# Optimization experiments

Hardware: AMD Instinct MI355X
Metric: run time of the kernel (lower is better)

Reference implementation:

```python
import jax, jax.numpy as jnp
import numpy as np
from jax import lax

HEADS = 8
DK = 128
DV = 128  # attention_channels


def circ_conv(x, w):
    # Conv2d with circular padding that preserves spatial size (odd kernel).
    k = w.shape[2]
    p = k // 2
    if p > 0:
        x = jnp.pad(x, ((0, 0), (0, 0), (p, p), (p, p)), mode='wrap')
    return lax.conv_general_dilated(x, w, (1, 1), 'VALID',
                                    dimension_numbers=('NCHW', 'OIHW', 'NCHW'))


def setup_inputs() -> dict:
    key = jax.random.key(0)
    k1, k2, k3, k4 = jax.random.split(key, 4)
    x = jax.random.normal(k1, (4, 128, 48, 48), dtype=jnp.float32)
    w_init = jax.random.normal(k2, (128, 128, 3, 3), dtype=jnp.float32) * 0.03
    w_qkv = jax.random.normal(k3, (384, 128, 3, 3), dtype=jnp.float32) * 0.03
    w_out = jax.random.normal(k4, (128, 128, 1, 1), dtype=jnp.float32) * 0.1
    return {"x": x, "w_init": w_init, "w_qkv": w_qkv, "w_out": w_out}


def reference(x, w_init, w_qkv, w_out):
    out = circ_conv(x, w_init)               # (b, out_ch - dv, h, w)
    b, _, H, W = out.shape
    N = H * W
    dk_h = DK // HEADS
    dv_h = DV // HEADS

    qkv = circ_conv(x, w_qkv)                # (b, 2*dk+dv, h, w)
    q, k, v = jnp.split(qkv, [DK, 2 * DK], axis=1)

    scale = dk_h ** (-0.5)
    fq = q.reshape(b, HEADS, dk_h, N) * scale
    fk = k.reshape(b, HEADS, dk_h, N)
    fv = v.reshape(b, HEADS, dv_h, N)

    logits = jnp.einsum('bhdn,bhdm->bhnm', fq, fk)     # (b,H,N,N)
    weights = jax.nn.softmax(logits, axis=-1)
    attn = jnp.einsum('bhnm,bhdm->bhnd', weights, fv)  # (b,H,N,dv_h)

    # Faithful to torch: raw reshape (b,H,N,dv_h) -> (b,H,dv_h,h,w)
    attn = attn.reshape(b, HEADS, dv_h, H, W)
    attn = attn.reshape(b, HEADS * dv_h, H, W)
    attn = circ_conv(attn, w_out)
    return jnp.concatenate([out, attn], axis=1)
```

## Files before the change

kernel.cpp:

```cpp
#include <hip/hip_runtime.h>

typedef __attribute__((ext_vector_type(8))) short short8;
typedef __attribute__((ext_vector_type(4))) short shortx4;
typedef __attribute__((ext_vector_type(4))) float floatx4;
typedef __attribute__((ext_vector_type(4))) _Float16 half4;
typedef __attribute__((ext_vector_type(2))) _Float16 half2v;

__device__ __forceinline__ short bf16_short(float f) {
    unsigned u = __builtin_bit_cast(unsigned, f);
    u = (u + 0x7fff + ((u >> 16) & 1)) >> 16;
    return (short)u;
}

__device__ __forceinline__ float fast_exp2(float x) {
#if __has_builtin(__builtin_amdgcn_exp2f)
    return __builtin_amdgcn_exp2f(x);
#else
    return __expf(x * 0.6931471805599453f);
#endif
}

__device__ __forceinline__ half4 pk4(float p0, float p1, float p2, float p3) {
#if __has_builtin(__builtin_amdgcn_cvt_pkrtz)
    half2v lo = __builtin_bit_cast(half2v, __builtin_amdgcn_cvt_pkrtz(p0, p1));
    half2v hi = __builtin_bit_cast(half2v, __builtin_amdgcn_cvt_pkrtz(p2, p3));
    half4 o; o[0] = lo[0]; o[1] = lo[1]; o[2] = hi[0]; o[3] = hi[1];
    return o;
#else
    half4 o; o[0] = (_Float16)p0; o[1] = (_Float16)p1;
    o[2] = (_Float16)p2; o[3] = (_Float16)p3;
    return o;
#endif
}

__global__ __launch_bounds__(256) void transform_w(
    const float* __restrict__ wi, const float* __restrict__ wq,
    const float* __restrict__ wo, const float* __restrict__ x,
    short* __restrict__ Wt, short* __restrict__ Wot, short* __restrict__ Xt)
{
    if (blockIdx.x < 2368) {
        int idx = blockIdx.x * 256 + threadIdx.x;
        if (idx < 589824) {
            int j  = idx & 7;
            int t1 = idx >> 3;
            int co = t1 & 127;
            int t2 = t1 >> 7;
            int chunk = t2 & 15;
            int t3 = t2 >> 4;
            int cog = t3 & 3;
            int tap = t3 >> 2;
            int ci = chunk * 8 + j;
            float v;
            if (cog == 0) v = wi[(co * 128 + ci) * 9 + tap];
            else          v = wq[((((cog - 1) * 128) + co) * 128 + ci) * 9 + tap];
            Wt[idx] = bf16_short(v);
        } else {
            int i2 = idx - 589824;
            int j  = i2 & 7;
            int co = (i2 >> 3) & 127;
            int chunk = i2 >> 10;
            int ci = chunk * 8 + j;
            Wot[i2] = bf16_short(wo[co * 128 + ci]);
        }
    } else {
        int xid = (blockIdx.x - 2368) * 256 + threadIdx.x;
        int col   = xid % 48;
        int row   = (xid / 48) % 48;
        int chunk = (xid / 2304) % 16;
        int b     = xid / 36864;
        const float* xs = x + ((b * 128 + chunk * 8) * 48 + row) * 48 + col;
        short8 o;
        #pragma unroll
        for (int j = 0; j < 8; ++j) o[j] = bf16_short(xs[j * 2304]);
        *(short8*)&Xt[(size_t)xid * 8] = o;
    }
}

__global__ __launch_bounds__(512) void conv_main(
    const short* __restrict__ Xt, const short* __restrict__ Wt,
    float* __restrict__ dout, _Float16* __restrict__ qT,
    _Float16* __restrict__ kT, _Float16* __restrict__ vA)
{
    const int y   = blockIdx.x;
    const int cog = blockIdx.y;
    const int b   = blockIdx.z;

    __shared__ short Xs[16 * 3 * 48 * 8];

    const int t = threadIdx.x;
    const int wave = t >> 6, lane = t & 63, quad = lane >> 4, l16 = lane & 15;
    const int wv = wave & 3;
    const int kk0 = (wave >> 2) * 2;

    const short* wA = Wt + (size_t)cog * 16384 + (wv * 32 + l16) * 8;

    short8 A[2][4];
    #pragma unroll
    for (int kk = 0; kk < 2; ++kk) {
        int chA = (kk0 + kk) * 4 + quad;
        A[0][kk * 2 + 0] = *(const short8*)(wA + chA * 1024);
        A[0][kk * 2 + 1] = *(const short8*)(wA + chA * 1024 + 128);
    }

    {
        const short* xtb = Xt + (size_t)b * 16 * 48 * 48 * 8;
        #pragma unroll
        for (int it = 0; it < 5; ++it) {
            int w = it * 512 + t;
            if (w < 2304) {
                int col   = w % 48;
                int row3  = (w / 48) % 3;
                int chunk = w / 144;
                int rowg  = y + row3 - 1;
                rowg = (rowg < 0) ? rowg + 48 : (rowg >= 48 ? rowg - 48 : rowg);
                short8 v = *(const short8*)&xtb[((chunk * 48 + rowg) * 48 + col) * 8];
                *(short8*)&Xs[((chunk * 3 + row3) * 48 + col) * 8] = v;
            }
        }
    }

    floatx4 acc[2][3];
    #pragma unroll
    for (int i = 0; i < 2; ++i)
        #pragma unroll
        for (int jn = 0; jn < 3; ++jn) acc[i][jn] = (floatx4){0.f, 0.f, 0.f, 0.f};

    __syncthreads();

    #pragma unroll
    for (int tap = 0; tap < 9; ++tap) {
        const int cur = tap & 1;
        if (tap < 8) {
            const short* wn = wA + (tap + 1) * 65536;
            #pragma unroll
            for (int kk = 0; kk < 2; ++kk) {
                int chA = (kk0 + kk) * 4 + quad;
                A[cur ^ 1][kk * 2 + 0] = *(const short8*)(wn + chA * 1024);
                A[cur ^ 1][kk * 2 + 1] = *(const short8*)(wn + chA * 1024 + 128);
            }
        }

        const int dy = tap / 3, dx = tap % 3;
        int colw[3];
        #pragma unroll
        for (int nt = 0; nt < 3; ++nt) {
            int c = nt * 16 + l16 + dx - 1;
            c = (c < 0) ? c + 48 : (c >= 48 ? c - 48 : c);
            colw[nt] = c;
        }

        #pragma unroll
        for (int kk = 0; kk < 2; ++kk) {
            int chA = (kk0 + kk) * 4 + quad;
            short8 a0 = A[cur][kk * 2 + 0];
            short8 a1 = A[cur][kk * 2 + 1];
            #pragma unroll
            for (int nt = 0; nt < 3; ++nt) {
                short8 bf = *(const short8*)&Xs[((chA * 3 + dy) * 48 + colw[nt]) * 8];
                acc[0][nt] = __builtin_amdgcn_mfma_f32_16x16x32_bf16(a0, bf, acc[0][nt], 0, 0, 0);
                acc[1][nt] = __builtin_amdgcn_mfma_f32_16x16x32_bf16(a1, bf, acc[1][nt], 0, 0, 0);
            }
        }
    }

    __syncthreads();
    float* Rs = (float*)Xs;
    if (wave >= 4) {
        float* dst = Rs + ((wave - 4) * 64 + lane) * 25;
        #pragma unroll
        for (int mt = 0; mt < 2; ++mt)
            #pragma unroll
            for (int nt = 0; nt < 3; ++nt)
                #pragma unroll
                for (int r = 0; r < 4; ++r) dst[(mt * 3 + nt) * 4 + r] = acc[mt][nt][r];
    }
    __syncthreads();
    if (wave >= 4) return;

    {
        const float* src = Rs + (wave * 64 + lane) * 25;
        #pragma unroll
        for (int mt = 0; mt < 2; ++mt)
            #pragma unroll
            for (int nt = 0; nt < 3; ++nt)
                #pragma unroll
                for (int r = 0; r < 4; ++r) acc[mt][nt][r] += src[(mt * 3 + nt) * 4 + r];
    }

    if (cog == 0) {
        #pragma unroll
        for (int mt = 0; mt < 2; ++mt)
            #pragma unroll
            for (int nt = 0; nt < 3; ++nt)
                #pragma unroll
                for (int r = 0; r < 4; ++r) {
                    int n    = y * 48 + nt * 16 + l16;
                    int co_l = wave * 32 + mt * 16 + quad * 4 + r;
                    dout[(b * 256 + co_l) * 2304 + n] = acc[mt][nt][r];
                }
    } else if (cog == 3) {
        #pragma unroll
        for (int mt = 0; mt < 2; ++mt) {
            int hh = wave * 2 + mt;
            #pragma unroll
            for (int nt = 0; nt < 3; ++nt) {
                int s = y * 3 + nt;
                _Float16* dst = vA + (((size_t)(b * 8 + hh) * 144 + s) * 16) * 16 + l16;
                #pragma unroll
                for (int r = 0; r < 4; ++r)
                    dst[(quad * 4 + r) * 16] = (_Float16)acc[mt][nt][r];
            }
        }
    } else {
        _Float16* dst = (cog == 1) ? qT : kT;
        const float scale = (cog == 1) ? 0.360673762f : 1.0f;
        #pragma unroll
        for (int mt = 0; mt < 2; ++mt) {
            int hh = wave * 2 + mt;
            #pragma unroll
            for (int nt = 0; nt < 3; ++nt) {
                int n = y * 48 + nt * 16 + l16;
                half4 o;
                #pragma unroll
                for (int r = 0; r < 4; ++r) o[r] = (_Float16)(acc[mt][nt][r] * scale);
                *(half4*)&dst[((b * 8 + hh) * 2304 + n) * 16 + quad * 4] = o;
            }
        }
    }
}

__global__ __launch_bounds__(256) void attn_kernel(
    const _Float16* __restrict__ qT, const _Float16* __restrict__ kT,
    const _Float16* __restrict__ vA, short* __restrict__ attnbuf)
{
    const int bh = blockIdx.y;
    const int n0 = blockIdx.x * 64;

    __shared__ float Red[4][4][64][5];

    const int t = threadIdx.x;
    const int wave = t >> 6, lane = t & 63, quad = lane >> 4, l16 = lane & 15;

    const _Float16* qTb = qT + (size_t)bh * 2304 * 16;
    const _Float16* kTb = kT + (size_t)bh * 2304 * 16;
    const _Float16* vAb = vA + (size_t)bh * 144 * 256;

    half4 qf[4];
    #pragma unroll
    for (int f = 0; f < 4; ++f)
        qf[f] = *(const half4*)(qTb + (n0 + f * 16 + l16) * 16 + quad * 4);

    floatx4 accA[4], accB[4];
    float lsum[4];
    #pragma unroll
    for (int f = 0; f < 4; ++f) {
        accA[f] = (floatx4){0.f,0.f,0.f,0.f};
        accB[f] = (floatx4){0.f,0.f,0.f,0.f};
        lsum[f] = 0.f;
    }

    const int mbase = wave * 576;
    const int sig0  = wave * 36;
    const int vofs  = l16 * 16 + quad * 4;

    half4 kfA = *(const half4*)(kTb + (mbase + l16) * 16 + quad * 4);
    half4 vfA = *(const half4*)(vAb + sig0 * 256 + vofs);
    half4 kfB = *(const half4*)(kTb + (mbase + 16 + l16) * 16 + quad * 4);
    half4 vfB = *(const half4*)(vAb + (sig0 + 1) * 256 + vofs);

    #pragma unroll 2
    for (int s = 0; s < 18; ++s) {
        half4 kA = kfA, vAc = vfA, kB = kfB, vBc = vfB;
        if (s < 17) {
            int m1 = mbase + (s + 1) * 32;
            int sg = sig0 + (s + 1) * 2;
            kfA = *(const half4*)(kTb + (m1 + l16) * 16 + quad * 4);
            vfA = *(const half4*)(vAb + sg * 256 + vofs);
            kfB = *(const half4*)(kTb + (m1 + 16 + l16) * 16 + quad * 4);
            vfB = *(const half4*)(vAb + (sg + 1) * 256 + vofs);
        }
        floatx4 z = {0.f,0.f,0.f,0.f};
        floatx4 stA[4], stB[4];
        #pragma unroll
        for (int f = 0; f < 4; ++f)
            stA[f] = __builtin_amdgcn_mfma_f32_16x16x16f16(kA, qf[f], z, 0, 0, 0);
        #pragma unroll
        for (int f = 0; f < 4; ++f)
            stB[f] = __builtin_amdgcn_mfma_f32_16x16x16f16(kB, qf[f], z, 0, 0, 0);

        #pragma unroll
        for (int f = 0; f < 4; ++f) {
            float a0 = fast_exp2(stA[f][0]);
            float a1 = fast_exp2(stA[f][1]);
            float a2 = fast_exp2(stA[f][2]);
            float a3 = fast_exp2(stA[f][3]);
            lsum[f] += (a0 + a1) + (a2 + a3);
            accA[f] = __builtin_amdgcn_mfma_f32_16x16x16f16(vAc, pk4(a0,a1,a2,a3), accA[f], 0, 0, 0);
        }
        #pragma unroll
        for (int f = 0; f < 4; ++f) {
            float b0 = fast_exp2(stB[f][0]);
            float b1 = fast_exp2(stB[f][1]);
            float b2 = fast_exp2(stB[f][2]);
            float b3 = fast_exp2(stB[f][3]);
            lsum[f] += (b0 + b1) + (b2 + b3);
            accB[f] = __builtin_amdgcn_mfma_f32_16x16x16f16(vBc, pk4(b0,b1,b2,b3), accB[f], 0, 0, 0);
        }
    }

    #pragma unroll
    for (int f = 0; f < 4; ++f) {
        lsum[f] += __shfl_xor(lsum[f], 16, 64);
        lsum[f] += __shfl_xor(lsum[f], 32, 64);
    }

    #pragma unroll
    for (int f = 0; f < 4; ++f) {
        #pragma unroll
        for (int r = 0; r < 4; ++r) Red[wave][f][lane][r] = accA[f][r] + accB[f][r];
        Red[wave][f][lane][4] = lsum[f];
    }
    __syncthreads();

    {
        const int f = wave;
        float tot[4] = {0.f, 0.f, 0.f, 0.f};
        float ls = 0.f;
        #pragma unroll
        for (int w = 0; w < 4; ++w) {
            #pragma unroll
            for (int r = 0; r < 4; ++r) tot[r] += Red[w][f][lane][r];
            ls += Red[w][f][lane][4];
        }
        float rinv = 1.0f / ls;
        shortx4 o;
        #pragma unroll
        for (int r = 0; r < 4; ++r) o[r] = bf16_short(tot[r] * rinv);
        int n = n0 + f * 16 + l16;
        *(shortx4*)&attnbuf[((size_t)bh * 2304 + n) * 16 + quad * 4] = o;
    }
}

__global__ __launch_bounds__(256) void conv1x1(
    const short* __restrict__ attnbuf, const short* __restrict__ Wot,
    float* __restrict__ dout)
{
    const int b    = blockIdx.y;
    const int col0 = blockIdx.x * 32;
    constexpr int RSA = 136;

    __shared__ short Wo[16 * 128 * 8];
    __shared__ short As[32 * RSA];

    const int t = threadIdx.x;
    {
        short8* dst = (short8*)Wo;
        const short8* src = (const short8*)Wot;
        #pragma unroll
        for (int it = 0; it < 8; ++it) dst[it * 256 + t] = src[it * 256 + t];
    }
    {
        const short* ab = attnbuf + b * 128 * 2304;
        #pragma unroll
        for (int it = 0; it < 8; ++it) {
            int e = it * 256 + t;
            int ci = e >> 4, cp = e & 15;
            unsigned v = *(const unsigned*)(ab + ci * 2304 + col0 + cp * 2);
            As[(cp * 2) * RSA + ci]     = (short)(v & 0xffff);
            As[(cp * 2 + 1) * RSA + ci] = (short)(v >> 16);
        }
    }
    __syncthreads();

    const int wave = t >> 6, lane = t & 63, quad = lane >> 4, l16 = lane & 15;
    floatx4 acc[2][2];
    #pragma unroll
    for (int i = 0; i < 2; ++i)
        #pragma unroll
        for (int j = 0; j < 2; ++j) acc[i][j] = (floatx4){0.f, 0.f, 0.f, 0.f};

    #pragma unroll
    for (int kk = 0; kk < 4; ++kk) {
        int chA = kk * 4 + quad;
        short8 a0 = *(const short8*)&Wo[(chA * 128 + wave * 32 + l16) * 8];
        short8 a1 = *(const short8*)&Wo[(chA * 128 + wave * 32 + 16 + l16) * 8];
        #pragma unroll
        for (int nt = 0; nt < 2; ++nt) {
            short8 bf = *(const short8*)&As[(nt * 16 + l16) * RSA + kk * 32 + quad * 8];
            acc[0][nt] = __builtin_amdgcn_mfma_f32_16x16x32_bf16(a0, bf, acc[0][nt], 0, 0, 0);
            acc[1][nt] = __builtin_amdgcn_mfma_f32_16x16x32_bf16(a1, bf, acc[1][nt], 0, 0, 0);
        }
    }

    #pragma unroll
    for (int mt = 0; mt < 2; ++mt)
        #pragma unroll
        for (int nt = 0; nt < 2; ++nt)
            #pragma unroll
            for (int r = 0; r < 4; ++r) {
                int co  = wave * 32 + mt * 16 + quad * 4 + r;
                int col = col0 + nt * 16 + l16;
                dout[(b * 256 + 128 + co) * 2304 + col] = acc[mt][nt][r];
            }
}

extern "C" void kernel_launch(void* const* d_in, const int* in_sizes, int n_in,
                              void* d_out, int out_size, void* d_ws, size_t ws_size,
                              hipStream_t stream)
{
    const float* x  = (const float*)d_in[0];
    const float* wi = (const float*)d_in[1];
    const float* wq = (const float*)d_in[2];
    const float* wo = (const float*)d_in[3];
    float* dout = (float*)d_out;

    char* ws = (char*)d_ws;
    _Float16* qT   = (_Float16*)(ws);
    _Float16* kT   = (_Float16*)(ws + 2359296);
    _Float16* vA   = (_Float16*)(ws + 4718592);
    short* attnbuf = (short*)(ws + 7077888);
    short* Wt      = (short*)(ws + 9437184);
    short* Wot     = (short*)(ws + 10616832);
    short* Xt      = (short*)(ws + 10649600);

    transform_w<<<2944, 256, 0, stream>>>(wi, wq, wo, x, Wt, Wot, Xt);
    conv_main<<<dim3(48, 4, 4), 512, 0, stream>>>(Xt, Wt, dout, qT, kT, vA);
    attn_kernel<<<dim3(36, 32), 256, 0, stream>>>(qT, kT, vA, attnbuf);
    conv1x1<<<dim3(72, 4), 256, 0, stream>>>(attnbuf, Wot, dout);
}
```

Before: 117.6 us.

## Write attention output in chunked channel layout and drop LDS staging in conv1x1

The weight transform now has each thread read the 9 contiguous taps of one (co,ci) pair instead of gathering strided elements, which cuts the block count for that part. The attention kernel writes its output directly in a channel-chunked (8-channel interleaved) layout that matches the MFMA B operand. This lets conv1x1 load fragments straight from global memory with no shared-memory transpose or barrier. The cost is scattered 2-byte stores in the attention epilogue in place of vectorized 8-byte stores.

```diff
diff --git a/kernel.cpp b/kernel.cpp
--- a/kernel.cpp
+++ b/kernel.cpp
@@ -38,32 +38,27 @@
     const float* __restrict__ wo, const float* __restrict__ x,
     short* __restrict__ Wt, short* __restrict__ Wot, short* __restrict__ Xt)
 {
-    if (blockIdx.x < 2368) {
+    if (blockIdx.x < 256) {
         int idx = blockIdx.x * 256 + threadIdx.x;
-        if (idx < 589824) {
-            int j  = idx & 7;
-            int t1 = idx >> 3;
-            int co = t1 & 127;
-            int t2 = t1 >> 7;
-            int chunk = t2 & 15;
-            int t3 = t2 >> 4;
-            int cog = t3 & 3;
-            int tap = t3 >> 2;
-            int ci = chunk * 8 + j;
-            float v;
-            if (cog == 0) v = wi[(co * 128 + ci) * 9 + tap];
-            else          v = wq[((((cog - 1) * 128) + co) * 128 + ci) * 9 + tap];
-            Wt[idx] = bf16_short(v);
-        } else {
-            int i2 = idx - 589824;
-            int j  = i2 & 7;
-            int co = (i2 >> 3) & 127;
-            int chunk = i2 >> 10;
-            int ci = chunk * 8 + j;
-            Wot[i2] = bf16_short(wo[co * 128 + ci]);
-        }
+        int ci  = idx & 127;
+        int cop = idx >> 7;
+        int cog = cop >> 7;
+        int co  = cop & 127;
+        const float* src = (cog == 0) ? (wi + (co * 128 + ci) * 9)
+                                      : (wq + (((cog - 1) * 128 + co) * 128 + ci) * 9);
+        int chunk = ci >> 3, j = ci & 7;
+        #pragma unroll
+        for (int tap = 0; tap < 9; ++tap)
+            Wt[((tap * 4 + cog) * 16 + chunk) * 1024 + co * 8 + j] = bf16_short(src[tap]);
+    } else if (blockIdx.x < 320) {
+        int i2 = (blockIdx.x - 256) * 256 + threadIdx.x;
+        int j  = i2 & 7;
+        int co = (i2 >> 3) & 127;
+        int chunk = i2 >> 10;
+        int ci = chunk * 8 + j;
+        Wot[i2] = bf16_short(wo[co * 128 + ci]);
     } else {
-        int xid = (blockIdx.x - 2368) * 256 + threadIdx.x;
+        int xid = (blockIdx.x - 320) * 256 + threadIdx.x;
         int col   = xid % 48;
         int row   = (xid / 48) % 48;
         int chunk = (xid / 2304) % 16;
@@ -231,9 +226,10 @@
 
 __global__ __launch_bounds__(256) void attn_kernel(
     const _Float16* __restrict__ qT, const _Float16* __restrict__ kT,
-    const _Float16* __restrict__ vA, short* __restrict__ attnbuf)
+    const _Float16* __restrict__ vA, short* __restrict__ Bb)
 {
     const int bh = blockIdx.y;
+    const int b = bh >> 3, h = bh & 7;
     const int n0 = blockIdx.x * 64;
 
     __shared__ float Red[4][4][64][5];
@@ -333,64 +329,57 @@
             ls += Red[w][f][lane][4];
         }
         float rinv = 1.0f / ls;
-        shortx4 o;
-        #pragma unroll
-        for (int r = 0; r < 4; ++r) o[r] = bf16_short(tot[r] * rinv);
         int n = n0 + f * 16 + l16;
-        *(shortx4*)&attnbuf[((size_t)bh * 2304 + n) * 16 + quad * 4] = o;
+        int c   = h * 16 + n / 144;
+        int col = (n % 144) * 16 + quad * 4;
+        short* dst = Bb + (size_t)b * 294912 + (c >> 3) * 18432 + col * 8 + (c & 7);
+        #pragma unroll
+        for (int r = 0; r < 4; ++r) dst[r * 8] = bf16_short(tot[r] * rinv);
     }
 }
 
 __global__ __launch_bounds__(256) void conv1x1(
-    const short* __restrict__ attnbuf, const short* __restrict__ Wot,
+    const short* __restrict__ Bb, const short* __restrict__ Wot,
     float* __restrict__ dout)
 {
     const int b    = blockIdx.y;
     const int col0 = blockIdx.x * 32;
-    constexpr int RSA = 136;
-
-    __shared__ short Wo[16 * 128 * 8];
-    __shared__ short As[32 * RSA];
 
     const int t = threadIdx.x;
-    {
-        short8* dst = (short8*)Wo;
-        const short8* src = (const short8*)Wot;
-        #pragma unroll
-        for (int it = 0; it < 8; ++it) dst[it * 256 + t] = src[it * 256 + t];
-    }
-    {
-        const short* ab = attnbuf + b * 128 * 2304;
-        #pragma unroll
-        for (int it = 0; it < 8; ++it) {
-            int e = it * 256 + t;
-            int ci = e >> 4, cp = e & 15;
-            unsigned v = *(const unsigned*)(ab + ci * 2304 + col0 + cp * 2);
-            As[(cp * 2) * RSA + ci]     = (short)(v & 0xffff);
-            As[(cp * 2 + 1) * RSA + ci] = (short)(v >> 16);
-        }
-    }
-    __syncthreads();
-
     const int wave = t >> 6, lane = t & 63, quad = lane >> 4, l16 = lane & 15;
-    floatx4 acc[2][2];
-    #pragma unroll
-    for (int i = 0; i < 2; ++i)
-        #pragma unroll
-        for (int j = 0; j < 2; ++j) acc[i][j] = (floatx4){0.f, 0.f, 0.f, 0.f};
-
+
+    short8 a[4][2];
     #pragma unroll
     for (int kk = 0; kk < 4; ++kk) {
         int chA = kk * 4 + quad;
-        short8 a0 = *(const short8*)&Wo[(chA * 128 + wave * 32 + l16) * 8];
-        short8 a1 = *(const short8*)&Wo[(chA * 128 + wave * 32 + 16 + l16) * 8];
+        const short* wp = Wot + (chA * 128 + wave * 32 + l16) * 8;
+        a[kk][0] = *(const short8*)wp;
+        a[kk][1] = *(const short8*)(wp + 128);
+    }
+
+    short8 bf[4][2];
+    #pragma unroll
+    for (int kk = 0; kk < 4; ++kk) {
+        int chA = kk * 4 + quad;
+        const short* bp = Bb + (size_t)b * 294912 + chA * 18432;
+        #pragma unroll
+        for (int nt = 0; nt < 2; ++nt)
+            bf[kk][nt] = *(const short8*)(bp + (col0 + nt * 16 + l16) * 8);
+    }
+
+    floatx4 acc[2][2];
+    #pragma unroll
+    for (int i = 0; i < 2; ++i)
+        #pragma unroll
+        for (int j = 0; j < 2; ++j) acc[i][j] = (floatx4){0.f, 0.f, 0.f, 0.f};
+
+    #pragma unroll
+    for (int kk = 0; kk < 4; ++kk)
         #pragma unroll
         for (int nt = 0; nt < 2; ++nt) {
-            short8 bf = *(const short8*)&As[(nt * 16 + l16) * RSA + kk * 32 + quad * 8];
-            acc[0][nt] = __builtin_amdgcn_mfma_f32_16x16x32_bf16(a0, bf, acc[0][nt], 0, 0, 0);
-            acc[1][nt] = __builtin_amdgcn_mfma_f32_16x16x32_bf16(a1, bf, acc[1][nt], 0, 0, 0);
-        }
-    }
+            acc[0][nt] = __builtin_amdgcn_mfma_f32_16x16x32_bf16(a[kk][0], bf[kk][nt], acc[0][nt], 0, 0, 0);
+            acc[1][nt] = __builtin_amdgcn_mfma_f32_16x16x32_bf16(a[kk][1], bf[kk][nt], acc[1][nt], 0, 0, 0);
+        }
 
     #pragma unroll
     for (int mt = 0; mt < 2; ++mt)
@@ -418,13 +407,13 @@
     _Float16* qT   = (_Float16*)(ws);
     _Float16* kT   = (_Float16*)(ws + 2359296);
     _Float16* vA   = (_Float16*)(ws + 4718592);
-    short* attnbuf = (short*)(ws + 7077888);
+    short* Bb      = (short*)(ws + 7077888);
     short* Wt      = (short*)(ws + 9437184);
     short* Wot     = (short*)(ws + 10616832);
     short* Xt      = (short*)(ws + 10649600);
 
-    transform_w<<<2944, 256, 0, stream>>>(wi, wq, wo, x, Wt, Wot, Xt);
+    transform_w<<<896, 256, 0, stream>>>(wi, wq, wo, x, Wt, Wot, Xt);
     conv_main<<<dim3(48, 4, 4), 512, 0, stream>>>(Xt, Wt, dout, qT, kT, vA);
-    attn_kernel<<<dim3(36, 32), 256, 0, stream>>>(qT, kT, vA, attnbuf);
-    conv1x1<<<dim3(72, 4), 256, 0, stream>>>(attnbuf, Wot, dout);
-}
+    attn_kernel<<<dim3(36, 32), 256, 0, stream>>>(qT, kT, vA, Bb);
+    conv1x1<<<dim3(72, 4), 256, 0, stream>>>(Bb, Wot, dout);
+}
```

After: 123.1 us. +4.6%, slower.
